# Performance work log

Measured on AMD Instinct MI355X. Metric: run time of the kernel, lower is better.

Reference implementation:

```python
import jax, jax.numpy as jnp
import numpy as np

N_NODES = 100000
N_EDGES = 1000000
D = 64
LN_EPS = 1e-5
DIV_EPS = 1e-6


def _layernorm(x, g, b):
    mu = x.mean(-1, keepdims=True)
    var = ((x - mu) ** 2).mean(-1, keepdims=True)
    return (x - mu) * jax.lax.rsqrt(var + LN_EPS) * g + b


def _linear_params(key, d_in, d_out):
    kw, kb = jax.random.split(key)
    s = 1.0 / np.sqrt(d_in)
    w = jax.random.uniform(kw, (d_in, d_out), jnp.float32, -s, s)
    b = jax.random.uniform(kb, (d_out,), jnp.float32, -s, s)
    return w, b


def setup_inputs() -> dict:
    key = jax.random.key(0)
    ks = jax.random.split(key, 10)
    h = jax.random.normal(ks[0], (N_NODES, D), jnp.float32)
    e = jax.random.normal(ks[1], (N_EDGES, D), jnp.float32)
    src = jax.random.randint(ks[2], (N_EDGES,), 0, N_NODES)
    dst = jax.random.randint(ks[3], (N_EDGES,), 0, N_NODES)
    A1w, A1b = _linear_params(ks[4], D, D)
    A2w, A2b = _linear_params(ks[5], D, D)
    B1w, B1b = _linear_params(ks[6], D, D)
    B2w, B2b = _linear_params(ks[7], D, D)
    B3w, B3b = _linear_params(ks[8], D, D)
    return {
        "h": h, "e": e, "src": src, "dst": dst,
        "A1w": A1w, "A1b": A1b, "A2w": A2w, "A2b": A2b,
        "B1w": B1w, "B1b": B1b, "B2w": B2w, "B2b": B2b,
        "B3w": B3w, "B3b": B3b,
        "ln_e_g": jnp.ones((D,), jnp.float32), "ln_e_b": jnp.zeros((D,), jnp.float32),
        "ln_h_g": jnp.ones((D,), jnp.float32), "ln_h_b": jnp.zeros((D,), jnp.float32),
    }


def reference(h, e, src, dst, A1w, A1b, A2w, A2b, B1w, B1b, B2w, B2b, B3w, B3b,
              ln_e_g, ln_e_b, ln_h_g, ln_h_b):
    # dense projections (small GEMMs, d=64)
    A1h = h @ A1w + A1b          # [N, D]
    A2h = h @ A2w + A2b          # [N, D]
    B1h = h @ B1w + B1b          # [N, D]
    B2h = h @ B2w + B2b          # [N, D]
    B3e = e @ B3w + B3b          # [E, D]

    # apply_edges u_add_v: B1h[src] + B2h[dst], plus B3e
    e_ji = B1h[src] + B2h[dst] + B3e            # [E, D]
    e_ji = jax.nn.relu(_layernorm(e_ji, ln_e_g, ln_e_b))
    e_ji = e_ji + e                              # residual (in==out)

    sigma = jax.nn.sigmoid(e_ji)                 # [E, D]

    # update_all u_mul_e sum: sum over incoming edges at dst of A2h[src]*sigma
    sum_sigma_h = jax.ops.segment_sum(A2h[src] * sigma, dst, num_segments=N_NODES)
    sum_sigma = jax.ops.segment_sum(sigma, dst, num_segments=N_NODES)

    h_forward = sum_sigma_h / (sum_sigma + DIV_EPS)
    h_out = jax.nn.relu(_layernorm(A1h + h_forward, ln_h_g, ln_h_b))
    h_out = h_out + h                            # residual
    return (h_out, e_ji)
```

## Files before the change

kernel.cpp:

```cpp
#include <hip/hip_runtime.h>

#define D 64
#define LN_EPS 1e-5f
#define DIV_EPS 1e-6f

typedef __attribute__((ext_vector_type(8))) short bf16x8;
typedef __attribute__((ext_vector_type(4))) float f32x4;

__device__ __forceinline__ short f2bf(float f) {
  unsigned u = __float_as_uint(f);
  unsigned r = (u + 0x7fffu + ((u >> 16) & 1u)) >> 16;
  return (short)r;
}

__device__ __forceinline__ f32x4 ntld4(const float* p) {
  return __builtin_nontemporal_load((const f32x4*)p);
}

__device__ __forceinline__ float gsum16(float v) {
#pragma unroll
  for (int m = 1; m < 16; m <<= 1) v += __shfl_xor(v, m, 64);
  return v;
}

__device__ __forceinline__ bf16x8 load_bfrag(const float* __restrict__ W,
                                             int s, int n0, int lane) {
  const int c = n0 * 16 + (lane & 15);
  const int k0 = s * 32 + ((lane >> 4) << 3);
  bf16x8 b;
#pragma unroll
  for (int j = 0; j < 8; ++j) b[j] = f2bf(W[(k0 + j) * D + c]);
  return b;
}

__device__ __forceinline__ void load_afrags(const float* __restrict__ X,
                                            size_t r0, int lane, bf16x8& a0,
                                            bf16x8& a1) {
  const int q = lane >> 4, m = lane & 15;
  const float* rb = X + (r0 + m) * D;
  const float4* p0 = (const float4*)(rb + q * 8);
  const float4* p1 = (const float4*)(rb + 32 + q * 8);
  float4 v0 = p0[0], v1 = p0[1], v2 = p1[0], v3 = p1[1];
  a0 = (bf16x8){f2bf(v0.x), f2bf(v0.y), f2bf(v0.z), f2bf(v0.w),
                f2bf(v1.x), f2bf(v1.y), f2bf(v1.z), f2bf(v1.w)};
  a1 = (bf16x8){f2bf(v2.x), f2bf(v2.y), f2bf(v2.z), f2bf(v2.w),
                f2bf(v3.x), f2bf(v3.y), f2bf(v3.z), f2bf(v3.w)};
}

__global__ __launch_bounds__(256) void node_proj2(
    const float* __restrict__ h, const float* __restrict__ W0,
    const float* __restrict__ Bb0, const float* __restrict__ W1,
    const float* __restrict__ Bb1, const float* __restrict__ W2,
    const float* __restrict__ Bb2, const float* __restrict__ W3,
    const float* __restrict__ Bb3, float* __restrict__ o0,
    float* __restrict__ o1, float* __restrict__ o2, float* __restrict__ o3,
    int N) {
  const int lane = threadIdx.x & 63;
  const int q = lane >> 4, m = lane & 15;
  const int wid = threadIdx.x >> 6;
  const float* Ws[4] = {W0, W1, W2, W3};
  const float* Bs[4] = {Bb0, Bb1, Bb2, Bb3};
  float* Os[4] = {o0, o1, o2, o3};
  const float* W = Ws[wid];
  float* Om = Os[wid];
  bf16x8 bf[2][4];
#pragma unroll
  for (int s = 0; s < 2; ++s)
#pragma unroll
    for (int n0 = 0; n0 < 4; ++n0) bf[s][n0] = load_bfrag(W, s, n0, lane);
  float bias[4];
#pragma unroll
  for (int n0 = 0; n0 < 4; ++n0) bias[n0] = Bs[wid][n0 * 16 + m];
  for (int r0 = blockIdx.x * 16; r0 < N; r0 += gridDim.x * 16) {
    bf16x8 a0, a1;
    load_afrags(h, (size_t)r0, lane, a0, a1);
    f32x4 acc[4];
#pragma unroll
    for (int n0 = 0; n0 < 4; ++n0) {
      acc[n0] = (f32x4){0.f, 0.f, 0.f, 0.f};
      acc[n0] =
          __builtin_amdgcn_mfma_f32_16x16x32_bf16(a0, bf[0][n0], acc[n0], 0, 0, 0);
      acc[n0] =
          __builtin_amdgcn_mfma_f32_16x16x32_bf16(a1, bf[1][n0], acc[n0], 0, 0, 0);
    }
#pragma unroll
    for (int n0 = 0; n0 < 4; ++n0)
#pragma unroll
      for (int r = 0; r < 4; ++r)
        Om[(size_t)(r0 + q * 4 + r) * D + n0 * 16 + m] = acc[n0][r] + bias[n0];
  }
}


__global__ __launch_bounds__(256) void hist_kernel(const int* __restrict__ dst,
                                                   int* __restrict__ cnt,
                                                   int E) {
  for (int i = blockIdx.x * blockDim.x + threadIdx.x; i < E;
       i += gridDim.x * blockDim.x)
    atomicAdd(&cnt[dst[i]], 1);
}

#define SCAN_B 256
__global__ __launch_bounds__(SCAN_B) void scan1(const int* __restrict__ cnt,
                                                int* __restrict__ rs,
                                                int* __restrict__ bsum, int n) {
  __shared__ int s[SCAN_B];
  const int i = blockIdx.x * SCAN_B + threadIdx.x;
  const int v = (i < n) ? cnt[i] : 0;
  s[threadIdx.x] = v;
  __syncthreads();
#pragma unroll
  for (int off = 1; off < SCAN_B; off <<= 1) {
    int t = (threadIdx.x >= off) ? s[threadIdx.x - off] : 0;
    __syncthreads();
    s[threadIdx.x] += t;
    __syncthreads();
  }
  if (i < n) rs[i] = s[threadIdx.x] - v;
  if (threadIdx.x == SCAN_B - 1) bsum[blockIdx.x] = s[SCAN_B - 1];
}

__global__ __launch_bounds__(512) void scan2(int* __restrict__ bsum, int nb) {
  __shared__ int s[512];
  const int v = (threadIdx.x < nb) ? bsum[threadIdx.x] : 0;
  s[threadIdx.x] = v;
  __syncthreads();
#pragma unroll
  for (int off = 1; off < 512; off <<= 1) {
    int t = (threadIdx.x >= off) ? s[threadIdx.x - off] : 0;
    __syncthreads();
    s[threadIdx.x] += t;
    __syncthreads();
  }
  if (threadIdx.x < nb) bsum[threadIdx.x] = s[threadIdx.x] - v;
}

__global__ __launch_bounds__(SCAN_B) void scan3(int* __restrict__ rs,
                                                int* __restrict__ cur,
                                                const int* __restrict__ bsum,
                                                int n, int E) {
  const int i = blockIdx.x * SCAN_B + threadIdx.x;
  if (i < n) {
    const int v = rs[i] + bsum[blockIdx.x];
    rs[i] = v;
    cur[i] = v;
  }
  if (blockIdx.x == 0 && threadIdx.x == 0) rs[n] = E;
}

__global__ __launch_bounds__(256) void place_kernel(const int* __restrict__ dst,
                                                    int* __restrict__ cur,
                                                    int* __restrict__ list,
                                                    int E) {
  for (int i = blockIdx.x * blockDim.x + threadIdx.x; i < E;
       i += gridDim.x * blockDim.x) {
    const int p = atomicAdd(&cur[dst[i]], 1);
    list[p] = i;
  }
}

__global__ __launch_bounds__(256, 4) void edge_mfma4(
    const float* __restrict__ e, const int* __restrict__ src,
    const int* __restrict__ dst, const float* __restrict__ B1h,
    const float* __restrict__ B2h, const float* __restrict__ W3,
    const float* __restrict__ B3b, const float* __restrict__ g,
    const float* __restrict__ bta, float* __restrict__ eout, int E) {
  __shared__ float es[4][16][68];
  const int lane = threadIdx.x & 63;
  const int q = lane >> 4, m = lane & 15;
  const int wid = threadIdx.x >> 6;
  const int gw = blockIdx.x * 4 + wid;
  const int nw = gridDim.x * 4;
  bf16x8 bf[2][4];
#pragma unroll
  for (int s = 0; s < 2; ++s)
#pragma unroll
    for (int n0 = 0; n0 < 4; ++n0) bf[s][n0] = load_bfrag(W3, s, n0, lane);
  float bb[4], gl[4], bl[4];
#pragma unroll
  for (int k = 0; k < 4; ++k) {
    const int c = m + 16 * k;
    bb[k] = B3b[c];
    gl[k] = g[c];
    bl[k] = bta[c];
  }
  for (int e0 = gw * 16; e0 < E; e0 += nw * 16) {
    const float* rb = e + (size_t)(e0 + m) * D;
    f32x4 v0 = ntld4(rb + q * 8);
    f32x4 v1 = ntld4(rb + q * 8 + 4);
    f32x4 v2 = ntld4(rb + 32 + q * 8);
    f32x4 v3 = ntld4(rb + 32 + q * 8 + 4);
    f32x4* erow = (f32x4*)&es[wid][m][0];
    erow[q * 2] = v0;
    erow[q * 2 + 1] = v1;
    erow[8 + q * 2] = v2;
    erow[8 + q * 2 + 1] = v3;
    bf16x8 a0 = (bf16x8){f2bf(v0[0]), f2bf(v0[1]), f2bf(v0[2]), f2bf(v0[3]),
                         f2bf(v1[0]), f2bf(v1[1]), f2bf(v1[2]), f2bf(v1[3])};
    bf16x8 a1 = (bf16x8){f2bf(v2[0]), f2bf(v2[1]), f2bf(v2[2]), f2bf(v2[3]),
                         f2bf(v3[0]), f2bf(v3[1]), f2bf(v3[2]), f2bf(v3[3])};
    f32x4 acc[4];
#pragma unroll
    for (int n0 = 0; n0 < 4; ++n0) {
      acc[n0] = (f32x4){0.f, 0.f, 0.f, 0.f};
      acc[n0] =
          __builtin_amdgcn_mfma_f32_16x16x32_bf16(a0, bf[0][n0], acc[n0], 0, 0, 0);
      acc[n0] =
          __builtin_amdgcn_mfma_f32_16x16x32_bf16(a1, bf[1][n0], acc[n0], 0, 0, 0);
    }
    const int sv = src[e0 + m];
    const int dv = dst[e0 + m];
#pragma unroll
    for (int r = 0; r < 4; ++r) {
      const int tr = q * 4 + r;
      const int sN = __shfl(sv, tr, 64);
      const int dN = __shfl(dv, tr, 64);
      const size_t sb = (size_t)sN * D, db = (size_t)dN * D;
      float x[4], part = 0.f;
#pragma unroll
      for (int k = 0; k < 4; ++k) {
        const int c = m + 16 * k;
        x[k] = acc[k][r] + bb[k] + B1h[sb + c] + B2h[db + c];
        part += x[k];
      }
      const float mu = gsum16(part) * (1.f / 64.f);
      float dx[4], vp = 0.f;
#pragma unroll
      for (int k = 0; k < 4; ++k) {
        dx[k] = x[k] - mu;
        vp += dx[k] * dx[k];
      }
      const float rs = rsqrtf(gsum16(vp) * (1.f / 64.f) + LN_EPS);
      const size_t eb = (size_t)(e0 + tr) * D;
#pragma unroll
      for (int k = 0; k < 4; ++k) {
        const int c = m + 16 * k;
        eout[eb + c] = fmaxf(dx[k] * rs * gl[k] + bl[k], 0.f) + es[wid][tr][c];
      }
    }
  }
}

__global__ __launch_bounds__(256) void aggregate_out(
    const float* __restrict__ h, const float* __restrict__ A1h,
    const float* __restrict__ A2h, const float* __restrict__ eout,
    const int* __restrict__ rs, const int* __restrict__ list,
    const int* __restrict__ src, const float* __restrict__ g,
    const float* __restrict__ bta, float* __restrict__ hout, int N) {
  const int lane = threadIdx.x & 63;
  const int q = lane >> 4, m = lane & 15;
  const int wave = blockIdx.x * 4 + (threadIdx.x >> 6);
  const int nw = gridDim.x * 4;
  const f32x4 gl = ((const f32x4*)g)[m];
  const f32x4 bl = ((const f32x4*)bta)[m];
  for (int n = wave * 4 + q; n < N; n += nw * 4) {
    const int s = rs[n], t = rs[n + 1];
    f32x4 acc0 = (f32x4){0.f, 0.f, 0.f, 0.f};
    f32x4 acc1 = (f32x4){0.f, 0.f, 0.f, 0.f};
    for (int b = s; b < t; b += 16) {
      const int nn = min(16, t - b);
      const int jm = (m < nn) ? list[b + m] : 0;
      const int sm = (m < nn) ? src[jm] : 0;
      for (int u = 0; u < nn; ++u) {
        const int jj = __shfl(jm, q * 16 + u, 64);
        const int sj = __shfl(sm, q * 16 + u, 64);
        const f32x4 y = *(const f32x4*)(eout + (size_t)jj * D + m * 4);
        const f32x4 a2 = *(const f32x4*)(A2h + (size_t)sj * D + m * 4);
#pragma unroll
        for (int k = 0; k < 4; ++k) {
          const float sg = 1.f / (1.f + __expf(-y[k]));
          acc0[k] += sg;
          acc1[k] += a2[k] * sg;
        }
      }
    }
    const size_t base = (size_t)n * D + m * 4;
    const f32x4 a1 = ntld4(A1h + base);
    const f32x4 hv = ntld4(h + base);
    float x[4], part = 0.f;
#pragma unroll
    for (int k = 0; k < 4; ++k) {
      x[k] = a1[k] + acc1[k] / (acc0[k] + DIV_EPS);
      part += x[k];
    }
    const float mu = gsum16(part) * (1.f / 64.f);
    float dx[4], vp = 0.f;
#pragma unroll
    for (int k = 0; k < 4; ++k) {
      dx[k] = x[k] - mu;
      vp += dx[k] * dx[k];
    }
    const float rsv = rsqrtf(gsum16(vp) * (1.f / 64.f) + LN_EPS);
    f32x4 y;
#pragma unroll
    for (int k = 0; k < 4; ++k)
      y[k] = fmaxf(dx[k] * rsv * gl[k] + bl[k], 0.f) + hv[k];
    __builtin_nontemporal_store(y, (f32x4*)(hout + base));
  }
}

extern "C" void kernel_launch(void* const* d_in, const int* in_sizes, int n_in,
                              void* d_out, int out_size, void* d_ws,
                              size_t ws_size, hipStream_t stream) {
  const float* h = (const float*)d_in[0];
  const float* e = (const float*)d_in[1];
  const int* src = (const int*)d_in[2];
  const int* dst = (const int*)d_in[3];
  const float* A1w = (const float*)d_in[4];
  const float* A1b = (const float*)d_in[5];
  const float* A2w = (const float*)d_in[6];
  const float* A2b = (const float*)d_in[7];
  const float* B1w = (const float*)d_in[8];
  const float* B1b = (const float*)d_in[9];
  const float* B2w = (const float*)d_in[10];
  const float* B2b = (const float*)d_in[11];
  const float* B3w = (const float*)d_in[12];
  const float* B3b = (const float*)d_in[13];
  const float* ln_e_g = (const float*)d_in[14];
  const float* ln_e_b = (const float*)d_in[15];
  const float* ln_h_g = (const float*)d_in[16];
  const float* ln_h_b = (const float*)d_in[17];

  const int N = in_sizes[0] / D;
  const int E = in_sizes[1] / D;

  float* ws = (float*)d_ws;
  float* A1h = ws;
  float* A2h = ws + (size_t)N * D;
  float* B1h = ws + 2 * (size_t)N * D;
  float* B2h = ws + 3 * (size_t)N * D;
  int* ip = (int*)(ws + 4 * (size_t)N * D);
  int* rs = ip;
  int* cur = ip + (N + 1);
  int* list = cur + N;
  int* bsum = list + E;

  float* hout = (float*)d_out;
  float* eout = (float*)d_out + (size_t)N * D;

  const int nb = (N + SCAN_B - 1) / SCAN_B;

  hipMemsetAsync(cur, 0, (size_t)N * sizeof(int), stream);

  node_proj2<<<3125, 256, 0, stream>>>(h, B1w, B1b, B2w, B2b, A1w, A1b, A2w,
                                       A2b, B1h, B2h, A1h, A2h, N);
  hist_kernel<<<512, 256, 0, stream>>>(dst, cur, E);
  scan1<<<nb, SCAN_B, 0, stream>>>(cur, rs, bsum, N);
  scan2<<<1, 512, 0, stream>>>(bsum, nb);
  scan3<<<nb, SCAN_B, 0, stream>>>(rs, cur, bsum, N, E);
  place_kernel<<<512, 256, 0, stream>>>(dst, cur, list, E);
  edge_mfma4<<<3907, 256, 0, stream>>>(e, src, dst, B1h, B2h, B3w, B3b, ln_e_g,
                                       ln_e_b, eout, E);
  aggregate_out<<<4096, 256, 0, stream>>>(h, A1h, A2h, eout, rs, list, src,
                                          ln_h_g, ln_h_b, hout, N);
}
```

Measured before the change: 793.5 us.

## Fuse sigmoid aggregation into edge kernel via dst-sorted order with run-length atomics

The edge kernel now walks edges in destination-sorted (CSR list) order and computes the edge LayerNorm output, its sigmoid, and the A2h-weighted sums in one pass. Partial sums for consecutive edges that share a destination are combined in registers and flushed to global sum buffers with atomics. This removes the second pass that re-read eout and A2h per edge. The histogram kernel is merged into the projection launch as extra blocks. In exchange, e rows are read in gathered rather than sequential order, float atomics make results order-dependent, and two extra N×D buffers must be zeroed.

New measurement: 804.9 us. Within noise of the previous version (+1.4%).

```diff
diff --git a/kernel.cpp b/kernel.cpp
--- a/kernel.cpp
+++ b/kernel.cpp
@@ -3,6 +3,9 @@
 #define D 64
 #define LN_EPS 1e-5f
 #define DIV_EPS 1e-6f
+#define PROJ_B 3125
+#define HIST_B 512
+#define SCAN_B 256
 
 typedef __attribute__((ext_vector_type(8))) short bf16x8;
 typedef __attribute__((ext_vector_type(4))) float f32x4;
@@ -47,14 +50,21 @@
                 f2bf(v3.x), f2bf(v3.y), f2bf(v3.z), f2bf(v3.w)};
 }
 
-__global__ __launch_bounds__(256) void node_proj2(
+__global__ __launch_bounds__(256) void proj_hist(
     const float* __restrict__ h, const float* __restrict__ W0,
     const float* __restrict__ Bb0, const float* __restrict__ W1,
     const float* __restrict__ Bb1, const float* __restrict__ W2,
     const float* __restrict__ Bb2, const float* __restrict__ W3,
     const float* __restrict__ Bb3, float* __restrict__ o0,
     float* __restrict__ o1, float* __restrict__ o2, float* __restrict__ o3,
-    int N) {
+    int N, const int* __restrict__ dst, int* __restrict__ cnt, int E) {
+  if (blockIdx.x >= PROJ_B) {
+    const int hb = blockIdx.x - PROJ_B;
+    const int nhb = gridDim.x - PROJ_B;
+    for (int i = hb * 256 + threadIdx.x; i < E; i += nhb * 256)
+      atomicAdd(&cnt[dst[i]], 1);
+    return;
+  }
   const int lane = threadIdx.x & 63;
   const int q = lane >> 4, m = lane & 15;
   const int wid = threadIdx.x >> 6;
@@ -71,7 +81,7 @@
   float bias[4];
 #pragma unroll
   for (int n0 = 0; n0 < 4; ++n0) bias[n0] = Bs[wid][n0 * 16 + m];
-  for (int r0 = blockIdx.x * 16; r0 < N; r0 += gridDim.x * 16) {
+  for (int r0 = blockIdx.x * 16; r0 < N; r0 += PROJ_B * 16) {
     bf16x8 a0, a1;
     load_afrags(h, (size_t)r0, lane, a0, a1);
     f32x4 acc[4];
@@ -92,15 +102,6 @@
 }
 
 
-__global__ __launch_bounds__(256) void hist_kernel(const int* __restrict__ dst,
-                                                   int* __restrict__ cnt,
-                                                   int E) {
-  for (int i = blockIdx.x * blockDim.x + threadIdx.x; i < E;
-       i += gridDim.x * blockDim.x)
-    atomicAdd(&cnt[dst[i]], 1);
-}
-
-#define SCAN_B 256
 __global__ __launch_bounds__(SCAN_B) void scan1(const int* __restrict__ cnt,
                                                 int* __restrict__ rs,
                                                 int* __restrict__ bsum, int n) {
@@ -159,12 +160,14 @@
   }
 }
 
-__global__ __launch_bounds__(256, 4) void edge_mfma4(
+__global__ __launch_bounds__(256, 4) void edge_csr(
     const float* __restrict__ e, const int* __restrict__ src,
-    const int* __restrict__ dst, const float* __restrict__ B1h,
-    const float* __restrict__ B2h, const float* __restrict__ W3,
+    const int* __restrict__ dst, const int* __restrict__ list,
+    const float* __restrict__ B1h, const float* __restrict__ B2h,
+    const float* __restrict__ A2h, const float* __restrict__ W3,
     const float* __restrict__ B3b, const float* __restrict__ g,
-    const float* __restrict__ bta, float* __restrict__ eout, int E) {
+    const float* __restrict__ bta, float* __restrict__ eout,
+    float* __restrict__ ssh, float* __restrict__ ss, int E) {
   __shared__ float es[4][16][68];
   const int lane = threadIdx.x & 63;
   const int q = lane >> 4, m = lane & 15;
@@ -184,103 +187,126 @@
     gl[k] = g[c];
     bl[k] = bta[c];
   }
-  for (int e0 = gw * 16; e0 < E; e0 += nw * 16) {
-    const float* rb = e + (size_t)(e0 + m) * D;
-    f32x4 v0 = ntld4(rb + q * 8);
-    f32x4 v1 = ntld4(rb + q * 8 + 4);
-    f32x4 v2 = ntld4(rb + 32 + q * 8);
-    f32x4 v3 = ntld4(rb + 32 + q * 8 + 4);
-    f32x4* erow = (f32x4*)&es[wid][m][0];
-    erow[q * 2] = v0;
-    erow[q * 2 + 1] = v1;
-    erow[8 + q * 2] = v2;
-    erow[8 + q * 2 + 1] = v3;
-    bf16x8 a0 = (bf16x8){f2bf(v0[0]), f2bf(v0[1]), f2bf(v0[2]), f2bf(v0[3]),
-                         f2bf(v1[0]), f2bf(v1[1]), f2bf(v1[2]), f2bf(v1[3])};
-    bf16x8 a1 = (bf16x8){f2bf(v2[0]), f2bf(v2[1]), f2bf(v2[2]), f2bf(v2[3]),
-                         f2bf(v3[0]), f2bf(v3[1]), f2bf(v3[2]), f2bf(v3[3])};
-    f32x4 acc[4];
-#pragma unroll
-    for (int n0 = 0; n0 < 4; ++n0) {
-      acc[n0] = (f32x4){0.f, 0.f, 0.f, 0.f};
-      acc[n0] =
-          __builtin_amdgcn_mfma_f32_16x16x32_bf16(a0, bf[0][n0], acc[n0], 0, 0, 0);
-      acc[n0] =
-          __builtin_amdgcn_mfma_f32_16x16x32_bf16(a1, bf[1][n0], acc[n0], 0, 0, 0);
-    }
-    const int sv = src[e0 + m];
-    const int dv = dst[e0 + m];
-#pragma unroll
-    for (int r = 0; r < 4; ++r) {
-      const int tr = q * 4 + r;
-      const int sN = __shfl(sv, tr, 64);
-      const int dN = __shfl(dv, tr, 64);
-      const size_t sb = (size_t)sN * D, db = (size_t)dN * D;
-      float x[4], part = 0.f;
+  for (int c0 = gw * 64; c0 < E; c0 += nw * 64) {
+    f32x4 r0a = (f32x4){0.f, 0.f, 0.f, 0.f};
+    f32x4 r1a = (f32x4){0.f, 0.f, 0.f, 0.f};
+    int d_run = -1;
+#pragma unroll
+    for (int t = 0; t < 4; ++t) {
+      const int p = c0 + ((m >> 2) << 4) + (t << 2) + (m & 3);
+      const bool pv = p < E;
+      const int jm = pv ? list[p] : 0;
+      const int sm = pv ? src[jm] : 0;
+      const int dm = pv ? dst[jm] : -1;
+      const float* rb = e + (size_t)jm * D;
+      f32x4 v0 = ntld4(rb + q * 8);
+      f32x4 v1 = ntld4(rb + q * 8 + 4);
+      f32x4 v2 = ntld4(rb + 32 + q * 8);
+      f32x4 v3 = ntld4(rb + 32 + q * 8 + 4);
+      f32x4* erow = (f32x4*)&es[wid][m][0];
+      erow[q * 2] = v0;
+      erow[q * 2 + 1] = v1;
+      erow[8 + q * 2] = v2;
+      erow[8 + q * 2 + 1] = v3;
+      bf16x8 a0 = (bf16x8){f2bf(v0[0]), f2bf(v0[1]), f2bf(v0[2]), f2bf(v0[3]),
+                           f2bf(v1[0]), f2bf(v1[1]), f2bf(v1[2]), f2bf(v1[3])};
+      bf16x8 a1 = (bf16x8){f2bf(v2[0]), f2bf(v2[1]), f2bf(v2[2]), f2bf(v2[3]),
+                           f2bf(v3[0]), f2bf(v3[1]), f2bf(v3[2]), f2bf(v3[3])};
+      f32x4 acc[4];
+#pragma unroll
+      for (int n0 = 0; n0 < 4; ++n0) {
+        acc[n0] = (f32x4){0.f, 0.f, 0.f, 0.f};
+        acc[n0] = __builtin_amdgcn_mfma_f32_16x16x32_bf16(a0, bf[0][n0],
+                                                          acc[n0], 0, 0, 0);
+        acc[n0] = __builtin_amdgcn_mfma_f32_16x16x32_bf16(a1, bf[1][n0],
+                                                          acc[n0], 0, 0, 0);
+      }
+#pragma unroll
+      for (int r = 0; r < 4; ++r) {
+        const int tr = q * 4 + r;
+        const int j = __shfl(jm, tr, 64);
+        const int sN = __shfl(sm, tr, 64);
+        const int dN = __shfl(dm, tr, 64);
+        if (dN < 0) continue;
+        const size_t sb = (size_t)sN * D, db = (size_t)dN * D;
+        float x[4], a2[4], part = 0.f;
+#pragma unroll
+        for (int k = 0; k < 4; ++k) {
+          const int c = m + 16 * k;
+          x[k] = acc[k][r] + bb[k] + B1h[sb + c] + B2h[db + c];
+          a2[k] = A2h[sb + c];
+          part += x[k];
+        }
+        const float mu = gsum16(part) * (1.f / 64.f);
+        float dx[4], vp = 0.f;
+#pragma unroll
+        for (int k = 0; k < 4; ++k) {
+          dx[k] = x[k] - mu;
+          vp += dx[k] * dx[k];
+        }
+        const float rsv = rsqrtf(gsum16(vp) * (1.f / 64.f) + LN_EPS);
+        const size_t eb = (size_t)j * D;
+        if (dN != d_run) {
+          if (d_run >= 0) {
+            const size_t fb = (size_t)d_run * D;
+#pragma unroll
+            for (int k = 0; k < 4; ++k) {
+              const int c = m + 16 * k;
+              atomicAdd(&ss[fb + c], r0a[k]);
+              atomicAdd(&ssh[fb + c], r1a[k]);
+            }
+          }
+          r0a = (f32x4){0.f, 0.f, 0.f, 0.f};
+          r1a = (f32x4){0.f, 0.f, 0.f, 0.f};
+          d_run = dN;
+        }
+#pragma unroll
+        for (int k = 0; k < 4; ++k) {
+          const int c = m + 16 * k;
+          const float y =
+              fmaxf(dx[k] * rsv * gl[k] + bl[k], 0.f) + es[wid][tr][c];
+          __builtin_nontemporal_store(y, eout + eb + c);
+          const float sg = 1.f / (1.f + __expf(-y));
+          r0a[k] += sg;
+          r1a[k] += a2[k] * sg;
+        }
+      }
+    }
+    if (d_run >= 0) {
+      const size_t fb = (size_t)d_run * D;
 #pragma unroll
       for (int k = 0; k < 4; ++k) {
         const int c = m + 16 * k;
-        x[k] = acc[k][r] + bb[k] + B1h[sb + c] + B2h[db + c];
-        part += x[k];
+        atomicAdd(&ss[fb + c], r0a[k]);
+        atomicAdd(&ssh[fb + c], r1a[k]);
       }
-      const float mu = gsum16(part) * (1.f / 64.f);
-      float dx[4], vp = 0.f;
-#pragma unroll
-      for (int k = 0; k < 4; ++k) {
-        dx[k] = x[k] - mu;
-        vp += dx[k] * dx[k];
-      }
-      const float rs = rsqrtf(gsum16(vp) * (1.f / 64.f) + LN_EPS);
-      const size_t eb = (size_t)(e0 + tr) * D;
-#pragma unroll
-      for (int k = 0; k < 4; ++k) {
-        const int c = m + 16 * k;
-        eout[eb + c] = fmaxf(dx[k] * rs * gl[k] + bl[k], 0.f) + es[wid][tr][c];
-      }
-    }
-  }
-}
-
-__global__ __launch_bounds__(256) void aggregate_out(
+    }
+  }
+}
+
+__global__ __launch_bounds__(256) void node_out2(
     const float* __restrict__ h, const float* __restrict__ A1h,
-    const float* __restrict__ A2h, const float* __restrict__ eout,
-    const int* __restrict__ rs, const int* __restrict__ list,
-    const int* __restrict__ src, const float* __restrict__ g,
-    const float* __restrict__ bta, float* __restrict__ hout, int N) {
+    const float* __restrict__ ssh, const float* __restrict__ ss,
+    const float* __restrict__ g, const float* __restrict__ bta,
+    float* __restrict__ hout, int n) {
   const int lane = threadIdx.x & 63;
   const int q = lane >> 4, m = lane & 15;
   const int wave = blockIdx.x * 4 + (threadIdx.x >> 6);
   const int nw = gridDim.x * 4;
   const f32x4 gl = ((const f32x4*)g)[m];
   const f32x4 bl = ((const f32x4*)bta)[m];
-  for (int n = wave * 4 + q; n < N; n += nw * 4) {
-    const int s = rs[n], t = rs[n + 1];
-    f32x4 acc0 = (f32x4){0.f, 0.f, 0.f, 0.f};
-    f32x4 acc1 = (f32x4){0.f, 0.f, 0.f, 0.f};
-    for (int b = s; b < t; b += 16) {
-      const int nn = min(16, t - b);
-      const int jm = (m < nn) ? list[b + m] : 0;
-      const int sm = (m < nn) ? src[jm] : 0;
-      for (int u = 0; u < nn; ++u) {
-        const int jj = __shfl(jm, q * 16 + u, 64);
-        const int sj = __shfl(sm, q * 16 + u, 64);
-        const f32x4 y = *(const f32x4*)(eout + (size_t)jj * D + m * 4);
-        const f32x4 a2 = *(const f32x4*)(A2h + (size_t)sj * D + m * 4);
-#pragma unroll
-        for (int k = 0; k < 4; ++k) {
-          const float sg = 1.f / (1.f + __expf(-y[k]));
-          acc0[k] += sg;
-          acc1[k] += a2[k] * sg;
-        }
-      }
-    }
-    const size_t base = (size_t)n * D + m * 4;
-    const f32x4 a1 = ntld4(A1h + base);
-    const f32x4 hv = ntld4(h + base);
+  for (int n0 = wave * 4; n0 < n; n0 += nw * 4) {
+    const int row = n0 + q;
+    if (row >= n) continue;
+    const size_t base = (size_t)row * D + m * 4;
+    f32x4 a1 = ntld4(A1h + base);
+    f32x4 s1 = ntld4(ssh + base);
+    f32x4 s2 = ntld4(ss + base);
+    f32x4 hv = ntld4(h + base);
     float x[4], part = 0.f;
 #pragma unroll
     for (int k = 0; k < 4; ++k) {
-      x[k] = a1[k] + acc1[k] / (acc0[k] + DIV_EPS);
+      x[k] = a1[k] + s1[k] / (s2[k] + DIV_EPS);
       part += x[k];
     }
     const float mu = gsum16(part) * (1.f / 64.f);
@@ -290,11 +316,11 @@
       dx[k] = x[k] - mu;
       vp += dx[k] * dx[k];
     }
-    const float rsv = rsqrtf(gsum16(vp) * (1.f / 64.f) + LN_EPS);
+    const float rs = rsqrtf(gsum16(vp) * (1.f / 64.f) + LN_EPS);
     f32x4 y;
 #pragma unroll
     for (int k = 0; k < 4; ++k)
-      y[k] = fmaxf(dx[k] * rsv * gl[k] + bl[k], 0.f) + hv[k];
+      y[k] = fmaxf(dx[k] * rs * gl[k] + bl[k], 0.f) + hv[k];
     __builtin_nontemporal_store(y, (f32x4*)(hout + base));
   }
 }
@@ -329,7 +355,9 @@
   float* A2h = ws + (size_t)N * D;
   float* B1h = ws + 2 * (size_t)N * D;
   float* B2h = ws + 3 * (size_t)N * D;
-  int* ip = (int*)(ws + 4 * (size_t)N * D);
+  float* ssh = ws + 4 * (size_t)N * D;
+  float* ss = ws + 5 * (size_t)N * D;
+  int* ip = (int*)(ws + 6 * (size_t)N * D);
   int* rs = ip;
   int* cur = ip + (N + 1);
   int* list = cur + N;
@@ -340,17 +368,17 @@
 
   const int nb = (N + SCAN_B - 1) / SCAN_B;
 
+  hipMemsetAsync(ssh, 0, 2 * (size_t)N * D * sizeof(float), stream);
   hipMemsetAsync(cur, 0, (size_t)N * sizeof(int), stream);
 
-  node_proj2<<<3125, 256, 0, stream>>>(h, B1w, B1b, B2w, B2b, A1w, A1b, A2w,
-                                       A2b, B1h, B2h, A1h, A2h, N);
-  hist_kernel<<<512, 256, 0, stream>>>(dst, cur, E);
+  proj_hist<<<PROJ_B + HIST_B, 256, 0, stream>>>(
+      h, B1w, B1b, B2w, B2b, A1w, A1b, A2w, A2b, B1h, B2h, A1h, A2h, N, dst,
+      cur, E);
   scan1<<<nb, SCAN_B, 0, stream>>>(cur, rs, bsum, N);
   scan2<<<1, 512, 0, stream>>>(bsum, nb);
   scan3<<<nb, SCAN_B, 0, stream>>>(rs, cur, bsum, N, E);
   place_kernel<<<512, 256, 0, stream>>>(dst, cur, list, E);
-  edge_mfma4<<<3907, 256, 0, stream>>>(e, src, dst, B1h, B2h, B3w, B3b, ln_e_g,
-                                       ln_e_b, eout, E);
-  aggregate_out<<<4096, 256, 0, stream>>>(h, A1h, A2h, eout, rs, list, src,
-                                          ln_h_g, ln_h_b, hout, N);
-}
+  edge_csr<<<3907, 256, 0, stream>>>(e, src, dst, list, B1h, B2h, A2h, B3w,
+                                     B3b, ln_e_g, ln_e_b, eout, ssh, ss, E);
+  node_out2<<<2048, 256, 0, stream>>>(h, A1h, ssh, ss, ln_h_g, ln_h_b, hout, N);
+}
```
